# Performance work log

Hardware: AMD Instinct MI355X
Metric: run time of the kernel (lower is better)

The kernel has to match this reference:

```python
import jax, jax.numpy as jnp
import numpy as np

SHIFTS = (1, 2)          # _GLOBAL_SHIFTS, all < channels so none filtered
LN_EPS = 1e-5


def _layernorm(x, g, b):
    mu = jnp.mean(x, axis=-1, keepdims=True)
    var = jnp.var(x, axis=-1, keepdims=True)
    return (x - mu) * jax.lax.rsqrt(var + LN_EPS) * g + b


def setup_inputs() -> dict:
    key = jax.random.key(0)
    ks = jax.random.split(key, 4)
    B, H, W, D = 8, 96, 96, 256
    n_comp = 2 * len(SHIFTS)  # full mode: dot + wedge per shift
    x = jax.random.normal(ks[0], (B, H, W, D), dtype=jnp.float32)
    # glorot-uniform style scaling for the two dense kernels
    pk = jax.random.normal(ks[1], (n_comp * D, D), dtype=jnp.float32) * (1.0 / np.sqrt(n_comp * D))
    gk = jax.random.normal(ks[2], (2 * D, D), dtype=jnp.float32) * (1.0 / np.sqrt(2 * D))
    return {
        "x": x,
        "ln_gamma": jnp.ones((D,), jnp.float32),
        "ln_beta": jnp.zeros((D,), jnp.float32),
        "proj_kernel": pk,
        "proj_bias": jnp.zeros((D,), jnp.float32),
        "gate_kernel": gk,
        "gate_bias": jnp.zeros((D,), jnp.float32),
        "gamma": jnp.full((D,), 1e-5, jnp.float32),  # LayerScale init
    }


def reference(x, ln_gamma, ln_beta, proj_kernel, proj_bias,
              gate_kernel, gate_bias, gamma):
    # ---- pre-norm ----
    h_norm = _layernorm(x, ln_gamma, ln_beta)                 # [B,H,W,D]
    # ---- context stream (ctx_mode='diff'): deviation from spatial mean ----
    z_det = h_norm
    z_ctx = h_norm - jnp.mean(h_norm, axis=(1, 2), keepdims=True)
    # ---- sparse rolling Clifford product (cli_mode='full') ----
    feats = []
    for s in SHIFTS:
        ctx_s = jnp.roll(z_ctx, -s, axis=-1)   # Z_ctx[(c+s) % D]
        det_s = jnp.roll(z_det, -s, axis=-1)   # Z_det[(c+s) % D]
        dot = jax.nn.silu(z_det * ctx_s)                      # inner part
        wedge = z_det * ctx_s - z_ctx * det_s                 # bivector part
        feats.append(dot)
        feats.append(wedge)
    feats = jnp.concatenate(feats, axis=-1)                   # [B,H,W,4D]
    g_feat = feats @ proj_kernel + proj_bias                  # [B,H,W,D]
    # ---- gated geometric residual ----
    gate_in = jnp.concatenate([h_norm, g_feat], axis=-1)      # [B,H,W,2D]
    alpha = jax.nn.sigmoid(gate_in @ gate_kernel + gate_bias)
    h_mix = (jax.nn.silu(h_norm) + alpha * g_feat) * gamma    # LayerScale
    # drop_path_rate == 0.0 -> identity; caller-side residual add
    return x + h_mix
```

## Files before the change

### kernel.cpp

```cpp
#include <hip/hip_runtime.h>
#include <hip/hip_bf16.h>

typedef unsigned short u16;
typedef unsigned int   u32;
typedef __attribute__((ext_vector_type(4))) float f32x4;
typedef __attribute__((ext_vector_type(4))) u32   u32x4;
typedef __attribute__((ext_vector_type(8))) short bf16x8;

#define HWPIX  9216
#define NPIX   73728
#define LN_EPS 1e-5f
#define MROW   64
#define HSTR   264
#define ASTR   40

template<int N> struct IC { static constexpr int value = N; };

__device__ __forceinline__ u16 f2bf(float f){
  u32 u = __builtin_bit_cast(u32, f);
  u += 0x7fffu + ((u >> 16) & 1u);
  return (u16)(u >> 16);
}
__device__ __forceinline__ u32 pkbf(float lo, float hi){
  u32 d;
  asm("v_cvt_pk_bf16_f32 %0, %1, %2" : "=v"(d) : "v"(lo), "v"(hi));
  return d;
}
__device__ __forceinline__ float lo2f(u32 w){ return __builtin_bit_cast(float, w << 16); }
__device__ __forceinline__ float hi2f(u32 w){ return __builtin_bit_cast(float, w & 0xffff0000u); }
__device__ __forceinline__ float bfu2f(u16 h){ return __builtin_bit_cast(float, (u32)h << 16); }
__device__ __forceinline__ float fsigmoid(float v){ return __fdividef(1.f, 1.f + __expf(-v)); }
__device__ __forceinline__ float fsilu(float v){ return __fdividef(v, 1.f + __expf(-v)); }

__global__ __launch_bounds__(256) void wconv(const float* __restrict__ pk,
                                             const float* __restrict__ gk,
                                             u16* __restrict__ wsdot,
                                             u16* __restrict__ wsgate)
{
  int gid = blockIdx.x * 256 + threadIdx.x;
  int t = gid >> 10, S = gid & 1023;
  int q = (S >> 2) & 15, pp = S & 3, w8 = (S >> 6) & 7, rb = S >> 9;
  int n  = rb * 128 + w8 * 16 + q;
  int kq = pp ^ ((q >> 1) & 3);
  const float* W; int k0; u16* dst;
  if (t < 8)       { W = pk; k0 =       t      * 32 + kq * 8; dst = wsdot  + (size_t)t * 8192; }
  else if (t < 16) { W = pk; k0 = 512 + (t-8)  * 32 + kq * 8; dst = wsdot  + (size_t)t * 8192; }
  else             { W = gk; k0 =       (t-16) * 32 + kq * 8; dst = wsgate + (size_t)(t-16) * 8192; }
  u32 ow[4];
  #pragma unroll
  for (int e = 0; e < 4; ++e) {
    float f0 = W[(size_t)(k0 + 2*e)     * 256 + n];
    float f1 = W[(size_t)(k0 + 2*e + 1) * 256 + n];
    ow[e] = (u32)f2bf(f0) | ((u32)f2bf(f1) << 16);
  }
  *(u32x4*)(dst + (size_t)S * 8) = (u32x4){ow[0], ow[1], ow[2], ow[3]};
}

__global__ __launch_bounds__(256) void ln_partial(const float* __restrict__ x,
                                                  const float* __restrict__ g,
                                                  const float* __restrict__ bt,
                                                  float* __restrict__ partial)
{
  const int bh = blockIdx.x;
  const int tid = threadIdx.x;
  const int wv = tid >> 6, lane = tid & 63;
  const float* xrow = x + (size_t)bh * 96 * 256;
  __shared__ float red[4][256];

  f32x4 gv = *(const f32x4*)(g  + lane * 4);
  f32x4 bv = *(const f32x4*)(bt + lane * 4);
  f32x4 acc = {0.f, 0.f, 0.f, 0.f};

  for (int w = wv; w < 96; w += 4) {
    f32x4 v = *(const f32x4*)(xrow + w * 256 + lane * 4);
    float s  = v[0] + v[1] + v[2] + v[3];
    float s2 = v[0]*v[0] + v[1]*v[1] + v[2]*v[2] + v[3]*v[3];
    #pragma unroll
    for (int m = 1; m < 64; m <<= 1) { s += __shfl_xor(s, m); s2 += __shfl_xor(s2, m); }
    float mu  = s * (1.f / 256.f);
    float var = s2 * (1.f / 256.f) - mu * mu;
    float rs  = rsqrtf(var + LN_EPS);
    #pragma unroll
    for (int j = 0; j < 4; ++j) acc[j] += (v[j] - mu) * rs * gv[j] + bv[j];
  }
  *(f32x4*)(&red[wv][lane * 4]) = acc;
  __syncthreads();
  float s = red[0][tid] + red[1][tid] + red[2][tid] + red[3][tid];
  partial[(size_t)bh * 256 + tid] = s;
}

__global__ __launch_bounds__(256) void ln_mean(const float* __restrict__ partial,
                                               float* __restrict__ mean)
{
  int b = blockIdx.x, c = threadIdx.x;
  float s = 0.f;
  for (int h = 0; h < 96; ++h) s += partial[((size_t)b * 96 + h) * 256 + c];
  float m = s * (1.f / 9216.f);
  mean[b * 258 + c] = m;
  if (c < 2) mean[b * 258 + 256 + c] = m;
}

__global__ __launch_bounds__(256) void wfold(const float* __restrict__ pk,
                                             const float* __restrict__ meang,
                                             u16* __restrict__ wsW)
{
  __shared__ float msh[256];
  int gid = blockIdx.x * 256 + threadIdx.x;
  int chunk = gid >> 10;
  int b = chunk >> 3, j = chunk & 7;
  msh[threadIdx.x] = meang[b * 258 + threadIdx.x];
  __syncthreads();
  int S = gid & 1023;
  int q = (S >> 2) & 15, pp = S & 3, w8 = (S >> 6) & 7, rb = S >> 9;
  int n  = rb * 128 + w8 * 16 + q;
  int kq = pp ^ ((q >> 1) & 3);
  u32 ow[4];
  #pragma unroll
  for (int e = 0; e < 4; ++e) {
    float r[2];
    #pragma unroll
    for (int hh = 0; hh < 2; ++hh) {
      int c = j * 32 + kq * 8 + 2 * e + hh;
      int cm1 = (c + 255) & 255, cm2 = (c + 254) & 255;
      int cp1 = (c + 1) & 255,   cp2 = (c + 2) & 255;
      r[hh] = msh[cm1] * pk[(size_t)(256 + cm1) * 256 + n]
            - msh[cp1] * pk[(size_t)(256 + c)   * 256 + n]
            + msh[cm2] * pk[(size_t)(768 + cm2) * 256 + n]
            - msh[cp2] * pk[(size_t)(768 + c)   * 256 + n];
    }
    ow[e] = (u32)f2bf(r[0]) | ((u32)f2bf(r[1]) << 16);
  }
  *(u32x4*)(wsW + (size_t)chunk * 8192 + (size_t)S * 8) = (u32x4){ow[0], ow[1], ow[2], ow[3]};
}

__global__ __launch_bounds__(512, 4) void fused(
    const float* __restrict__ x,
    const float* __restrict__ lng, const float* __restrict__ lnb,
    const u16* __restrict__ wsdot, const u16* __restrict__ wsW,
    const u16* __restrict__ wsgate,
    const float* __restrict__ pbias, const float* __restrict__ gbias,
    const float* __restrict__ gamma, const float* __restrict__ meang,
    float* __restrict__ out)
{
  __shared__ u16 hn[MROW * HSTR];
  __shared__ u16 afg[2][MROW * ASTR];
  __shared__ u16 Bl [2][8192];
  __shared__ float msh[258];

  const int tid  = threadIdx.x;
  const long pix0 = (long)blockIdx.x * MROW;
  const int bat  = (int)(pix0 / HWPIX);

  const int wave = tid >> 6, lane = tid & 63;
  const int wr = wave & 1, wc = wave >> 1;
  const int fr = lane & 15, kq = lane >> 4;
  const int bswz = (kq ^ ((fr >> 1) & 3)) * 8;
  const int br = tid >> 3, bo = (tid & 7) * 4;

  f32x4 acc[2][4];
  #pragma unroll
  for (int i = 0; i < 2; ++i)
    #pragma unroll
    for (int j = 0; j < 4; ++j) acc[i][j] = (f32x4){0.f, 0.f, 0.f, 0.f};
  u32 gfp[2][4][2];

  u32x4 brA0, brA1, brB0, brB1;
  auto sgptr = [&](auto SG) -> const u16* {
    constexpr int sg = decltype(SG)::value;
    if constexpr      (sg == 0) return wsdot;
    else if constexpr (sg == 1) return wsdot + 8 * 8192;
    else if constexpr (sg == 2) return wsW + (size_t)bat * 65536;
    else if constexpr (sg == 3) return wsgate;
    else                        return wsgate + 8 * 8192;
  };
  auto loadB = [&](auto SG, int jn, auto SET) {
    const u16* src = sgptr(SG) + (size_t)jn * 8192 + tid * 8;
    if constexpr (decltype(SET)::value == 0) {
      brA0 = *(const u32x4*)(src);
      brA1 = *(const u32x4*)(src + 4096);
    } else {
      brB0 = *(const u32x4*)(src);
      brB1 = *(const u32x4*)(src + 4096);
    }
  };
  auto writeB = [&](auto SET, int buf) {
    if constexpr (decltype(SET)::value == 0) {
      *(u32x4*)(&Bl[buf][tid * 8])        = brA0;
      *(u32x4*)(&Bl[buf][tid * 8 + 4096]) = brA1;
    } else {
      *(u32x4*)(&Bl[buf][tid * 8])        = brB0;
      *(u32x4*)(&Bl[buf][tid * 8 + 4096]) = brB1;
    }
  };

  loadB(IC<0>{}, 0, IC<0>{});
  loadB(IC<0>{}, 1, IC<1>{});

  if (tid < 258) msh[tid] = meang[bat * 258 + tid];

  float pbv[4];
  #pragma unroll
  for (int nt = 0; nt < 4; ++nt) pbv[nt] = pbias[wc * 64 + nt * 16 + fr];

  {
    const int p = tid >> 3, o = tid & 7;
    const float* xp = x + (pix0 + p) * 256 + o * 32;
    float s = 0.f, s2 = 0.f;
    #pragma unroll
    for (int i = 0; i < 8; ++i) {
      f32x4 v = *(const f32x4*)(xp + i * 4);
      s  += v[0] + v[1] + v[2] + v[3];
      s2 += v[0]*v[0] + v[1]*v[1] + v[2]*v[2] + v[3]*v[3];
    }
    s += __shfl_xor(s, 1); s2 += __shfl_xor(s2, 1);
    s += __shfl_xor(s, 2); s2 += __shfl_xor(s2, 2);
    s += __shfl_xor(s, 4); s2 += __shfl_xor(s2, 4);
    float mu  = s * (1.f / 256.f);
    float var = s2 * (1.f / 256.f) - mu * mu;
    float rs  = rsqrtf(var + LN_EPS);

    const float* gp = lng + o * 32;
    const float* bp = lnb + o * 32;
    u16* zd = hn + p * HSTR + o * 32;
    #pragma unroll
    for (int i = 0; i < 8; ++i) {
      f32x4 v  = *(const f32x4*)(xp + i * 4);
      f32x4 gg = *(const f32x4*)(gp + i * 4);
      f32x4 bb = *(const f32x4*)(bp + i * 4);
      float h0 = (v[0] - mu) * rs * gg[0] + bb[0];
      float h1 = (v[1] - mu) * rs * gg[1] + bb[1];
      float h2 = (v[2] - mu) * rs * gg[2] + bb[2];
      float h3 = (v[3] - mu) * rs * gg[3] + bb[3];
      u32 d0 = pkbf(h0, h1);
      u32 d1 = pkbf(h2, h3);
      *(u32*)(zd + i * 4)     = d0;
      *(u32*)(zd + i * 4 + 2) = d1;
      if (i == 0 && o == 0) *(u32*)(hn + p * HSTR + 256) = d0;
    }
  }

  auto featsD = [&](auto SC, int w, int buf) {
    constexpr int s = decltype(SC)::value;
    const int cc = w * 32 + bo;
    const u16* zp = hn + br * HSTR + cc;
    u32 a0 = *(const u32*)(zp);
    u32 a1 = *(const u32*)(zp + 2);
    u32 a2 = *(const u32*)(zp + 4);
    float h0 = lo2f(a0), h1 = hi2f(a0), h2 = lo2f(a1);
    float h3 = hi2f(a1), h4 = lo2f(a2), h5 = hi2f(a2);
    float m0 = msh[cc + s], m1 = msh[cc + s + 1];
    float m2 = msh[cc + s + 2], m3 = msh[cc + s + 3];
    float t0, t1, t2, t3;
    if constexpr (s == 1) { t0 = h1; t1 = h2; t2 = h3; t3 = h4; }
    else                  { t0 = h2; t1 = h3; t2 = h4; t3 = h5; }
    float r0 = fsilu(h0 * (t0 - m0));
    float r1 = fsilu(h1 * (t1 - m1));
    float r2 = fsilu(h2 * (t2 - m2));
    float r3 = fsilu(h3 * (t3 - m3));
    *(u32*)(&afg[buf][br * ASTR + bo])     = pkbf(r0, r1);
    *(u32*)(&afg[buf][br * ASTR + bo + 2]) = pkbf(r2, r3);
  };

  auto gfcopy = [&](auto CGC, int buf) {
    constexpr int cg = decltype(CGC)::value;
    constexpr int par = cg & 1;
    if (wc == (cg >> 1)) {
      #pragma unroll
      for (int v = 0; v < 2; ++v) {
        #pragma unroll
        for (int ai = 0; ai < 2; ++ai)
          #pragma unroll
          for (int rp = 0; rp < 2; ++rp) {
            u32 pw = gfp[ai][par * 2 + v][rp];
            int row0 = wr * 32 + ai * 16 + kq * 4 + rp * 2;
            afg[buf][row0 * ASTR + v * 16 + fr]       = (u16)pw;
            afg[buf][(row0 + 1) * ASTR + v * 16 + fr] = (u16)(pw >> 16);
          }
      }
    }
  };

  auto domfma = [&](const u16* abase, int astr, int buf) {
    bf16x8 av0 = *(const bf16x8*)(abase);
    bf16x8 av1 = *(const bf16x8*)(abase + 16 * astr);
    const u16* bp = &Bl[buf][wc * 2048 + fr * 32 + bswz];
    #pragma unroll
    for (int nt = 0; nt < 4; ++nt) {
      bf16x8 bv = *(const bf16x8*)(bp + nt * 512);
      acc[0][nt] = __builtin_amdgcn_mfma_f32_16x16x32_bf16(av0, bv, acc[0][nt], 0, 0, 0);
      acc[1][nt] = __builtin_amdgcn_mfma_f32_16x16x32_bf16(av1, bv, acc[1][nt], 0, 0, 0);
    }
  };

  __syncthreads();
  writeB(IC<0>{}, 0);
  featsD(IC<1>{}, 0, 0);
  __syncthreads();

  auto stepfn = [&](auto SEGC, auto JC) {
    constexpr int SEG = decltype(SEGC)::value;
    constexpr int j   = decltype(JC)::value;
    constexpr int t   = SEG * 8 + j;
    constexpr int cb  = t & 1, nb = cb ^ 1;
    constexpr int l   = t + 2;
    if constexpr (l < 40) loadB(IC<(l >> 3)>{}, l & 7, IC<l & 1>{});
    if constexpr (SEG == 0 || SEG == 1 || SEG == 4)
      domfma(&afg[cb][(wr * 32 + fr) * ASTR + kq * 8], ASTR, cb);
    else
      domfma(&hn[(wr * 32 + fr) * HSTR + j * 32 + kq * 8], HSTR, cb);
    constexpr int u    = t + 1;
    constexpr int useg = u >> 3;
    if constexpr (u < 40) {
      if constexpr      (useg == 0) featsD(IC<1>{}, u & 7, nb);
      else if constexpr (useg == 1) featsD(IC<2>{}, u & 7, nb);
      else if constexpr (useg == 4) gfcopy(IC<u - 32>{}, nb);
      writeB(IC<u & 1>{}, nb);
    }
    if constexpr (t == 23) {
      #pragma unroll
      for (int nt = 0; nt < 4; ++nt)
        #pragma unroll
        for (int ai = 0; ai < 2; ++ai) {
          f32x4 a = acc[ai][nt];
          gfp[ai][nt][0] = pkbf(a[0] + pbv[nt], a[1] + pbv[nt]);
          gfp[ai][nt][1] = pkbf(a[2] + pbv[nt], a[3] + pbv[nt]);
          acc[ai][nt] = (f32x4){0.f, 0.f, 0.f, 0.f};
        }
    }
    __syncthreads();
  };
  auto runseg = [&](auto SEGC) {
    stepfn(SEGC, IC<0>{}); stepfn(SEGC, IC<1>{});
    stepfn(SEGC, IC<2>{}); stepfn(SEGC, IC<3>{});
    stepfn(SEGC, IC<4>{}); stepfn(SEGC, IC<5>{});
    stepfn(SEGC, IC<6>{}); stepfn(SEGC, IC<7>{});
  };
  runseg(IC<0>{}); runseg(IC<1>{}); runseg(IC<2>{});
  runseg(IC<3>{}); runseg(IC<4>{});

  float gbv[4], gmv[4];
  #pragma unroll
  for (int nt = 0; nt < 4; ++nt) {
    int col = wc * 64 + nt * 16 + fr;
    gbv[nt] = gbias[col]; gmv[nt] = gamma[col];
  }
  #pragma unroll
  for (int ai = 0; ai < 2; ++ai)
    #pragma unroll
    for (int rr = 0; rr < 4; ++rr) {
      const int row = wr * 32 + ai * 16 + kq * 4 + rr;
      const long pix = pix0 + row;
      #pragma unroll
      for (int nt = 0; nt < 4; ++nt) {
        int col = wc * 64 + nt * 16 + fr;
        float xv = x[pix * 256 + col];
        float hh = bfu2f(hn[row * HSTR + col]);
        u32 pw = gfp[ai][nt][rr >> 1];
        float gfv = bfu2f((u16)((rr & 1) ? (pw >> 16) : pw));
        float al = fsigmoid(acc[ai][nt][rr] + gbv[nt]);
        out[pix * 256 + col] = xv + (fsilu(hh) + al * gfv) * gmv[nt];
      }
    }
}

extern "C" void kernel_launch(void* const* d_in, const int* in_sizes, int n_in,
                              void* d_out, int out_size, void* d_ws, size_t ws_size,
                              hipStream_t stream) {
  const float* x     = (const float*)d_in[0];
  const float* lng   = (const float*)d_in[1];
  const float* lnb   = (const float*)d_in[2];
  const float* pk    = (const float*)d_in[3];
  const float* pbias = (const float*)d_in[4];
  const float* gk    = (const float*)d_in[5];
  const float* gbias = (const float*)d_in[6];
  const float* gamma = (const float*)d_in[7];
  float* out = (float*)d_out;

  char* ws = (char*)d_ws;
  u16*   wsdot   = (u16*)ws;
  u16*   wsgate  = (u16*)(ws + 262144);
  float* meang   = (float*)(ws + 524288);
  u16*   wsW     = (u16*)(ws + 532544);
  float* partial = (float*)(ws + 532544);

  wconv<<<128, 256, 0, stream>>>(pk, gk, wsdot, wsgate);
  ln_partial<<<768, 256, 0, stream>>>(x, lng, lnb, partial);
  ln_mean<<<8, 256, 0, stream>>>(partial, meang);
  wfold<<<256, 256, 0, stream>>>(pk, meang, wsW);
  fused<<<NPIX / MROW, 512, 0, stream>>>(x, lng, lnb, wsdot, wsW, wsgate,
                                         pbias, gbias, gamma, meang, out);
}
```

Measured before the change: 150.8 us.

## Stage weight tiles directly into LDS with global_load_lds and raise MFMA priority

Replaces the register round-trip B-tile prefetch (global load into VGPRs two steps ahead, then an LDS write) with direct global-to-LDS async loads one step ahead into the next buffer, with explicit waitcnt plus barrier in place of __syncthreads. The aim is to cut VGPR pressure and LDS-write instructions and to overlap the weight fetch with compute. It also wraps the MFMA loop in s_setprio and widens one feature LDS read. The prefetch distance drops from two steps to one, so global latency is less hidden, and the vmcnt(0) wait at every step may stall.

```diff
diff --git a/kernel.cpp b/kernel.cpp
--- a/kernel.cpp
+++ b/kernel.cpp
@@ -3,6 +3,7 @@
 
 typedef unsigned short u16;
 typedef unsigned int   u32;
+typedef __attribute__((ext_vector_type(2))) u32   u32x2;
 typedef __attribute__((ext_vector_type(4))) float f32x4;
 typedef __attribute__((ext_vector_type(4))) u32   u32x4;
 typedef __attribute__((ext_vector_type(8))) short bf16x8;
@@ -31,6 +32,12 @@
 __device__ __forceinline__ float bfu2f(u16 h){ return __builtin_bit_cast(float, (u32)h << 16); }
 __device__ __forceinline__ float fsigmoid(float v){ return __fdividef(1.f, 1.f + __expf(-v)); }
 __device__ __forceinline__ float fsilu(float v){ return __fdividef(v, 1.f + __expf(-v)); }
+
+__device__ __forceinline__ void gld16(const u16* g, u16* l){
+  __builtin_amdgcn_global_load_lds((const __attribute__((address_space(1))) void*)g,
+                                   (__attribute__((address_space(3))) void*)l,
+                                   16, 0, 0);
+}
 
 __global__ __launch_bounds__(256) void wconv(const float* __restrict__ pk,
                                              const float* __restrict__ gk,
@@ -164,7 +171,6 @@
     for (int j = 0; j < 4; ++j) acc[i][j] = (f32x4){0.f, 0.f, 0.f, 0.f};
   u32 gfp[2][4][2];
 
-  u32x4 brA0, brA1, brB0, brB1;
   auto sgptr = [&](auto SG) -> const u16* {
     constexpr int sg = decltype(SG)::value;
     if constexpr      (sg == 0) return wsdot;
@@ -173,28 +179,15 @@
     else if constexpr (sg == 3) return wsgate;
     else                        return wsgate + 8 * 8192;
   };
-  auto loadB = [&](auto SG, int jn, auto SET) {
-    const u16* src = sgptr(SG) + (size_t)jn * 8192 + tid * 8;
-    if constexpr (decltype(SET)::value == 0) {
-      brA0 = *(const u32x4*)(src);
-      brA1 = *(const u32x4*)(src + 4096);
-    } else {
-      brB0 = *(const u32x4*)(src);
-      brB1 = *(const u32x4*)(src + 4096);
-    }
-  };
-  auto writeB = [&](auto SET, int buf) {
-    if constexpr (decltype(SET)::value == 0) {
-      *(u32x4*)(&Bl[buf][tid * 8])        = brA0;
-      *(u32x4*)(&Bl[buf][tid * 8 + 4096]) = brA1;
-    } else {
-      *(u32x4*)(&Bl[buf][tid * 8])        = brB0;
-      *(u32x4*)(&Bl[buf][tid * 8 + 4096]) = brB1;
-    }
-  };
-
-  loadB(IC<0>{}, 0, IC<0>{});
-  loadB(IC<0>{}, 1, IC<1>{});
+  auto stageB = [&](auto UC, int buf) {
+    constexpr int u = decltype(UC)::value;
+    const u16* src = sgptr(IC<(u >> 3)>{}) + (size_t)(u & 7) * 8192 + tid * 8;
+    u16* dst = &Bl[buf][wave * 512];
+    gld16(src, dst);
+    gld16(src + 4096, dst + 4096);
+  };
+
+  stageB(IC<0>{}, 0);
 
   if (tid < 258) msh[tid] = meang[bat * 258 + tid];
 
@@ -243,11 +236,10 @@
     constexpr int s = decltype(SC)::value;
     const int cc = w * 32 + bo;
     const u16* zp = hn + br * HSTR + cc;
-    u32 a0 = *(const u32*)(zp);
-    u32 a1 = *(const u32*)(zp + 2);
-    u32 a2 = *(const u32*)(zp + 4);
-    float h0 = lo2f(a0), h1 = hi2f(a0), h2 = lo2f(a1);
-    float h3 = hi2f(a1), h4 = lo2f(a2), h5 = hi2f(a2);
+    u32x2 aa = *(const u32x2*)(zp);
+    u32 a2   = *(const u32*)(zp + 4);
+    float h0 = lo2f(aa[0]), h1 = hi2f(aa[0]), h2 = lo2f(aa[1]);
+    float h3 = hi2f(aa[1]), h4 = lo2f(a2), h5 = hi2f(a2);
     float m0 = msh[cc + s], m1 = msh[cc + s + 1];
     float m2 = msh[cc + s + 2], m3 = msh[cc + s + 3];
     float t0, t1, t2, t3;
@@ -284,37 +276,38 @@
     bf16x8 av0 = *(const bf16x8*)(abase);
     bf16x8 av1 = *(const bf16x8*)(abase + 16 * astr);
     const u16* bp = &Bl[buf][wc * 2048 + fr * 32 + bswz];
+    __builtin_amdgcn_s_setprio(1);
     #pragma unroll
     for (int nt = 0; nt < 4; ++nt) {
       bf16x8 bv = *(const bf16x8*)(bp + nt * 512);
       acc[0][nt] = __builtin_amdgcn_mfma_f32_16x16x32_bf16(av0, bv, acc[0][nt], 0, 0, 0);
       acc[1][nt] = __builtin_amdgcn_mfma_f32_16x16x32_bf16(av1, bv, acc[1][nt], 0, 0, 0);
     }
-  };
-
-  __syncthreads();
-  writeB(IC<0>{}, 0);
+    __builtin_amdgcn_s_setprio(0);
+  };
+
+  asm volatile("s_waitcnt vmcnt(0) lgkmcnt(0)" ::: "memory");
+  __builtin_amdgcn_s_barrier();
   featsD(IC<1>{}, 0, 0);
-  __syncthreads();
+  asm volatile("s_waitcnt lgkmcnt(0)" ::: "memory");
+  __builtin_amdgcn_s_barrier();
 
   auto stepfn = [&](auto SEGC, auto JC) {
     constexpr int SEG = decltype(SEGC)::value;
     constexpr int j   = decltype(JC)::value;
     constexpr int t   = SEG * 8 + j;
     constexpr int cb  = t & 1, nb = cb ^ 1;
-    constexpr int l   = t + 2;
-    if constexpr (l < 40) loadB(IC<(l >> 3)>{}, l & 7, IC<l & 1>{});
+    constexpr int u   = t + 1;
+    if constexpr (u < 40) stageB(IC<u>{}, nb);
     if constexpr (SEG == 0 || SEG == 1 || SEG == 4)
       domfma(&afg[cb][(wr * 32 + fr) * ASTR + kq * 8], ASTR, cb);
     else
       domfma(&hn[(wr * 32 + fr) * HSTR + j * 32 + kq * 8], HSTR, cb);
-    constexpr int u    = t + 1;
     constexpr int useg = u >> 3;
     if constexpr (u < 40) {
       if constexpr      (useg == 0) featsD(IC<1>{}, u & 7, nb);
       else if constexpr (useg == 1) featsD(IC<2>{}, u & 7, nb);
       else if constexpr (useg == 4) gfcopy(IC<u - 32>{}, nb);
-      writeB(IC<u & 1>{}, nb);
     }
     if constexpr (t == 23) {
       #pragma unroll
@@ -327,7 +320,8 @@
           acc[ai][nt] = (f32x4){0.f, 0.f, 0.f, 0.f};
         }
     }
-    __syncthreads();
+    asm volatile("s_waitcnt vmcnt(0) lgkmcnt(0)" ::: "memory");
+    __builtin_amdgcn_s_barrier();
   };
   auto runseg = [&](auto SEGC) {
     stepfn(SEGC, IC<0>{}); stepfn(SEGC, IC<1>{});
```

New measurement: 154.9 us. 1.03x slower.
